# Optimization experiments

Hardware: AMD Instinct MI355X
Metric: run time of the kernel (lower is better)

## Reference

```python
import jax, jax.numpy as jnp
import numpy as np

B, S, DMODEL, HEADS = 2, 2048, 1024, 16
DK = DMODEL // HEADS
DV = DMODEL // HEADS


def setup_inputs() -> dict:
    key = jax.random.key(0)
    kx, kq, kk, kv = jax.random.split(key, 4)
    x = jax.random.normal(kx, (B, S, DMODEL), dtype=jnp.float32)
    # stacked per-head projection weights, shape [H, dmodel, dk/dv]
    # (equivalent to nn.Linear(dmodel, dk, bias=False) per head)
    scale = 1.0 / np.sqrt(DMODEL)
    Wq = jax.random.uniform(kq, (HEADS, DMODEL, DK), jnp.float32, -scale, scale)
    Wk = jax.random.uniform(kk, (HEADS, DMODEL, DK), jnp.float32, -scale, scale)
    Wv = jax.random.uniform(kv, (HEADS, DMODEL, DV), jnp.float32, -scale, scale)
    return {"x": x, "Wq": Wq, "Wk": Wk, "Wv": Wv}


def reference(x, Wq, Wk, Wv):
    # per-head projections, batched across heads: [B,H,S,dk]
    q = jnp.einsum("bsd,hdk->bhsk", x, Wq)
    k = jnp.einsum("bsd,hdk->bhsk", x, Wk)
    v = jnp.einsum("bsd,hdv->bhsv", x, Wv)
    # NOTE: original module applies NO 1/sqrt(dk) scaling — keep faithful
    scores = jnp.einsum("bhqk,bhsk->bhqs", q, k)  # [B,H,S,S]
    attn = jax.nn.softmax(scores, axis=-1)
    out = jnp.einsum("bhqs,bhsv->bhqv", attn, v)  # [B,H,S,dv]
    # concat heads along last dim in head order
    Bsz, H, Sq, Dv = out.shape
    return jnp.transpose(out, (0, 2, 1, 3)).reshape(Bsz, Sq, H * Dv)
```

## Files before the change

kernel.cpp:

```cpp
#include <hip/hip_runtime.h>

#define B_ 2
#define S_ 2048
#define D_ 1024
#define H_ 16
#define DK_ 64
#define M_ (B_ * S_)
#define N_ (3 * D_)

typedef __bf16 bf16x8 __attribute__((ext_vector_type(8)));
typedef short s8vec __attribute__((ext_vector_type(8)));
typedef float f4vec __attribute__((ext_vector_type(4)));
typedef float f16vec __attribute__((ext_vector_type(16)));

static __device__ __forceinline__ ushort f2b(float f) {
  union { float f; unsigned u; } v; v.f = f;
  unsigned u = v.u;
  u += 0x7FFFu + ((u >> 16) & 1u);
  return (ushort)(u >> 16);
}

static __device__ __forceinline__ unsigned pk2(float a, float b) {
#if __has_builtin(__builtin_amdgcn_cvt_pk_bf16_f32)
  typedef __bf16 b2 __attribute__((ext_vector_type(2)));
  b2 r = __builtin_amdgcn_cvt_pk_bf16_f32(a, b);
  return __builtin_bit_cast(unsigned, r);
#else
  return (unsigned)f2b(a) | ((unsigned)f2b(b) << 16);
#endif
}

static __device__ __forceinline__ float exp2f_fast(float x) {
#if __has_builtin(__builtin_amdgcn_exp2f)
  return __builtin_amdgcn_exp2f(x);
#else
  return __expf(x * 0.6931471805599453f);
#endif
}

static __device__ __forceinline__ f4vec mfma16(s8vec a, s8vec b, f4vec c) {
  return __builtin_amdgcn_mfma_f32_16x16x32_bf16(
      __builtin_bit_cast(bf16x8, a), __builtin_bit_cast(bf16x8, b), c, 0, 0, 0);
}

static __device__ __forceinline__ f16vec mfma32(s8vec a, s8vec b, f16vec c) {
  return __builtin_amdgcn_mfma_f32_32x32x16_bf16(
      __builtin_bit_cast(bf16x8, a), __builtin_bit_cast(bf16x8, b), c, 0, 0, 0);
}

static __device__ __forceinline__ void gl_lds16(const ushort* g, ushort* l) {
  __builtin_amdgcn_global_load_lds(
      (const __attribute__((address_space(1))) unsigned*)g,
      (__attribute__((address_space(3))) unsigned*)l, 16, 0, 0);
}

__global__ __launch_bounds__(256) void cvt_xw(const float* __restrict__ x,
                                              const float* __restrict__ Wq,
                                              const float* __restrict__ Wk,
                                              const float* __restrict__ Wv,
                                              ushort* __restrict__ xb,
                                              ushort* __restrict__ wbt) {
  __shared__ ushort T[64 * 72];
  const int t = threadIdx.x;
  if (blockIdx.x < 4096) {
    int i = blockIdx.x * 256 + t;
    float4 v = ((const float4*)x)[i];
    ushort4 o;
    o.x = f2b(v.x); o.y = f2b(v.y); o.z = f2b(v.z); o.w = f2b(v.w);
    ((ushort4*)xb)[i] = o;
    return;
  }
  const int r = blockIdx.x - 4096;
  const int w = r >> 8, h = (r >> 4) & 15, d0 = (r & 15) * 64;
  const float* W = (w == 0) ? Wq : (w == 1) ? Wk : Wv;
  const float sc = (w == 0) ? 1.4426950408889634f : 1.0f;
  const float* src = W + (size_t)h * 65536 + (size_t)d0 * 64;
#pragma unroll
  for (int j = 0; j < 4; ++j) {
    int idx = j * 256 + t;
    int dr = idx >> 4, kc = (idx & 15) * 4;
    float4 v = *(const float4*)(src + dr * 64 + kc);
    T[(kc + 0) * 72 + dr] = f2b(v.x * sc);
    T[(kc + 1) * 72 + dr] = f2b(v.y * sc);
    T[(kc + 2) * 72 + dr] = f2b(v.z * sc);
    T[(kc + 3) * 72 + dr] = f2b(v.w * sc);
  }
  __syncthreads();
  const int kk = t >> 2, dcg = (t & 3) * 16;
  ushort* dst = wbt + ((size_t)w * 1024 + h * 64 + kk) * 1024 + d0 + dcg;
  *(s8vec*)dst       = *(const s8vec*)&T[kk * 72 + dcg];
  *(s8vec*)(dst + 8) = *(const s8vec*)&T[kk * 72 + dcg + 8];
}

__global__ __launch_bounds__(512) void proj_gemm(const ushort* __restrict__ xb,
                                                 const ushort* __restrict__ wbt,
                                                 ushort* __restrict__ qkv) {
  __shared__ __attribute__((aligned(16))) ushort As[2][256 * 64];
  __shared__ __attribute__((aligned(16))) ushort Bs[2][192 * 64];
  const int tid = threadIdx.x, wid = tid >> 6, lane = tid & 63;
  const int quad = lane >> 4, l15 = lane & 15;
  const int wm = wid & 1, wn = wid >> 1;
  const int m0 = blockIdx.x * 256, n0 = blockIdx.y * 192;

  f4vec acc[8][3];
#pragma unroll
  for (int mb = 0; mb < 8; mb++)
#pragma unroll
    for (int nb = 0; nb < 3; nb++)
#pragma unroll
      for (int i = 0; i < 4; i++) acc[mb][nb][i] = 0.f;

  const int sr = tid >> 3, sg = tid & 7;
  const int gk = sg ^ (sr & 7) ^ ((sr >> 3) & 7);
  const ushort* Ab = xb + (size_t)m0 * D_;
  const ushort* Bb = wbt + (size_t)n0 * D_;

#define PSTAGE(buf, k0_)                                                    \
  do {                                                                      \
    _Pragma("unroll")                                                       \
    for (int j = 0; j < 4; ++j)                                             \
      gl_lds16(Ab + (size_t)(j * 64 + sr) * D_ + (k0_) + gk * 8,            \
               &As[buf][(j * 64 + wid * 8) * 64]);                          \
    _Pragma("unroll")                                                       \
    for (int j = 0; j < 3; ++j)                                             \
      gl_lds16(Bb + (size_t)(j * 64 + sr) * D_ + (k0_) + gk * 8,            \
               &Bs[buf][(j * 64 + wid * 8) * 64]);                          \
  } while (0)

#define PCOMP(buf)                                                          \
  do {                                                                      \
    _Pragma("unroll")                                                       \
    for (int kb = 0; kb < 2; ++kb) {                                        \
      s8vec af[8], bf[3];                                                   \
      _Pragma("unroll")                                                     \
      for (int mb = 0; mb < 8; ++mb) {                                      \
        int m = wm * 128 + mb * 16 + l15;                                   \
        int gpos = (kb * 4 + quad) ^ (m & 7) ^ ((mb * 2 + (l15 >> 3)) & 7); \
        af[mb] = *(const s8vec*)&As[buf][m * 64 + gpos * 8];                \
      }                                                                     \
      _Pragma("unroll")                                                     \
      for (int nb = 0; nb < 3; ++nb) {                                      \
        int n = wn * 48 + nb * 16 + l15;                                    \
        int gpos = (kb * 4 + quad) ^ (n & 7) ^                              \
                   ((wn * 6 + nb * 2 + (l15 >> 3)) & 7);                    \
        bf[nb] = *(const s8vec*)&Bs[buf][n * 64 + gpos * 8];                \
      }                                                                     \
      _Pragma("unroll")                                                     \
      for (int mb = 0; mb < 8; ++mb)                                        \
        _Pragma("unroll")                                                   \
        for (int nb = 0; nb < 3; ++nb)                                      \
          acc[mb][nb] = mfma16(af[mb], bf[nb], acc[mb][nb]);                \
    }                                                                       \
  } while (0)

  PSTAGE(0, 0);
  __syncthreads();
  for (int t = 0; t < 15; ++t) {
    const int cur = t & 1;
    PSTAGE(cur ^ 1, (t + 1) * 64);
    PCOMP(cur);
    __syncthreads();
  }
  PCOMP(1);
#undef PSTAGE
#undef PCOMP

  const size_t per = (size_t)B_ * H_ * S_ * DK_;
  ushort* vt = qkv + 2 * per;
#pragma unroll
  for (int mb = 0; mb < 8; ++mb)
#pragma unroll
    for (int nb = 0; nb < 3; ++nb) {
      const int n1g = n0 + wn * 48 + nb * 16 + l15;
      const int w = n1g >> 10, n1 = n1g & 1023;
      if (w == 2) {
#pragma unroll
        for (int i = 0; i < 4; ++i) {
          int m = m0 + wm * 128 + mb * 16 + quad * 4 + i;
          int b = m >> 11, s = m & 2047;
          vt[((size_t)b * 1024 + n1) * S_ + s] = f2b(acc[mb][nb][i]);
        }
      } else {
#pragma unroll
        for (int i = 0; i < 4; ++i) {
          int m = m0 + wm * 128 + mb * 16 + quad * 4 + i;
          int b = m >> 11, s = m & 2047;
          qkv[(size_t)w * per + (((size_t)b * H_ + (n1 >> 6)) * S_ + s) * 64 + (n1 & 63)] =
              f2b(acc[mb][nb][i]);
        }
      }
    }
}

__global__ __launch_bounds__(512) void attn(const ushort* __restrict__ qg,
                                            const ushort* __restrict__ kg,
                                            const ushort* __restrict__ vtg,
                                            float* __restrict__ out) {
  __shared__ __attribute__((aligned(16))) ushort POOL[2][128 * 64 + 2 * 64 * 64];
  __shared__ float LM[4][32];
  float* OM = (float*)POOL;

  const int L = blockIdx.x + (blockIdx.y << 4);
  const int orig = (L & 7) * 64 + (L >> 3);
  const int qt = orig & 15, bh = orig >> 4;
  const int b = bh >> 4, h = bh & 15;
  const int tid = threadIdx.x, wid = tid >> 6, lane = tid & 63;
  const int l31 = lane & 31, hi = lane >> 5, l7 = lane & 7;
  const int j3 = l31 >> 3;
  const int qgi = wid >> 1, kh = wid & 1;

  const ushort* qb = qg + ((size_t)bh * S_ + qt * 128 + qgi * 32) * DK_;
  s8vec bq[4];
#pragma unroll
  for (int s = 0; s < 4; ++s)
    bq[s] = *(const s8vec*)(qb + (size_t)l31 * DK_ + s * 16 + hi * 8);

  f16vec o[2];
  float lsum = 0.f;
#pragma unroll
  for (int dvh = 0; dvh < 2; ++dvh)
#pragma unroll
    for (int i = 0; i < 16; ++i) o[dvh][i] = 0.f;

  const int srow = wid * 8 + (lane >> 3);
  const int gk = (lane & 7) ^ ((lane >> 3) & 7) ^ wid;
  const ushort* kb_ = kg + (size_t)bh * S_ * DK_;
  const ushort* vb_ = vtg + (size_t)bh * 64 * S_ + (size_t)srow * S_;

#define STAGE(buf, kt_)                                                     \
  do {                                                                      \
    const ushort* kk0 = kb_ + (size_t)((kt_) * 128 + srow) * DK_ + gk * 8;  \
    gl_lds16(kk0, &POOL[buf][wid * 512]);                                   \
    gl_lds16(kk0 + (size_t)64 * DK_, &POOL[buf][4096 + wid * 512]);         \
    gl_lds16(vb_ + (kt_) * 128 + gk * 8, &POOL[buf][8192 + wid * 512]);     \
    gl_lds16(vb_ + (kt_) * 128 + 64 + gk * 8,                               \
             &POOL[buf][8192 + 4096 + wid * 512]);                          \
  } while (0)

  STAGE(0, 0);
  __syncthreads();

  for (int kt = 0; kt < S_ / 128; ++kt) {
    const int cur = kt & 1;
    if (kt + 1 < S_ / 128) STAGE(cur ^ 1, kt + 1);

    const ushort* ksb = POOL[cur];
    const ushort* vtb = POOL[cur] + 8192;
#pragma unroll
    for (int c = 0; c < 2; ++c) {
      const int row0 = kh * 64 + c * 32 + l31;
      const int akx = l7 ^ ((c * 4 + j3) & 7);
      s8vec ak[4];
#pragma unroll
      for (int s = 0; s < 4; ++s)
        ak[s] = *(const s8vec*)&ksb[row0 * 64 + ((2 * s + hi) ^ akx) * 8];

      f16vec st;
#pragma unroll
      for (int i = 0; i < 16; ++i) st[i] = 0.f;
      __builtin_amdgcn_s_setprio(1);
#pragma unroll
      for (int s = 0; s < 4; ++s) st = mfma32(ak[s], bq[s], st);
      __builtin_amdgcn_s_setprio(0);

      float p[16];
#pragma unroll
      for (int r = 0; r < 16; ++r) p[r] = exp2f_fast(st[r]);
      lsum += (((p[0] + p[1]) + (p[2] + p[3])) + ((p[4] + p[5]) + (p[6] + p[7]))) +
              (((p[8] + p[9]) + (p[10] + p[11])) + ((p[12] + p[13]) + (p[14] + p[15])));
#pragma unroll
      for (int m = 0; m < 2; ++m) {
        unsigned u01 = pk2(p[m * 8 + 0], p[m * 8 + 1]);
        unsigned u23 = pk2(p[m * 8 + 2], p[m * 8 + 3]);
        unsigned u89 = pk2(p[m * 8 + 4], p[m * 8 + 5]);
        unsigned uAB = pk2(p[m * 8 + 6], p[m * 8 + 7]);
        asm("v_permlane32_swap_b32 %0, %1" : "+v"(u01), "+v"(u89));
        asm("v_permlane32_swap_b32 %0, %1" : "+v"(u23), "+v"(uAB));
        union { unsigned u[4]; s8vec v; } pb;
        pb.u[0] = u01; pb.u[1] = u23; pb.u[2] = u89; pb.u[3] = uAB;
        __builtin_amdgcn_s_setprio(1);
#pragma unroll
        for (int dvh = 0; dvh < 2; ++dvh) {
          s8vec av = *(const s8vec*)&vtb[kh * 4096 + (dvh * 32 + l31) * 64 +
                                         (((4 * c + 2 * m + hi) ^ l7 ^
                                           ((dvh * 4 + j3) & 7)) * 8)];
          o[dvh] = mfma32(av, pb.v, o[dvh]);
        }
        __builtin_amdgcn_s_setprio(0);
      }
    }
    __syncthreads();
  }
#undef STAGE

  lsum += __shfl_xor(lsum, 32, 64);

  if (kh == 1) {
#pragma unroll
    for (int dvh = 0; dvh < 2; ++dvh)
#pragma unroll
      for (int r = 0; r < 16; ++r)
        OM[(qgi * 2 + dvh) * 2048 + r * 64 + lane] = o[dvh][r];
    if (!hi) LM[qgi][l31] = lsum;
  }
  __syncthreads();
  if (kh == 0) {
    const float linv = 1.0f / (lsum + LM[qgi][l31]);
    float* ob = out + ((size_t)b * S_ + qt * 128 + qgi * 32) * D_ + h * DK_;
#pragma unroll
    for (int dvh = 0; dvh < 2; ++dvh)
#pragma unroll
      for (int qd = 0; qd < 4; ++qd) {
        float4 vv;
        vv.x = (o[dvh][qd * 4 + 0] + OM[(qgi * 2 + dvh) * 2048 + (qd * 4 + 0) * 64 + lane]) * linv;
        vv.y = (o[dvh][qd * 4 + 1] + OM[(qgi * 2 + dvh) * 2048 + (qd * 4 + 1) * 64 + lane]) * linv;
        vv.z = (o[dvh][qd * 4 + 2] + OM[(qgi * 2 + dvh) * 2048 + (qd * 4 + 2) * 64 + lane]) * linv;
        vv.w = (o[dvh][qd * 4 + 3] + OM[(qgi * 2 + dvh) * 2048 + (qd * 4 + 3) * 64 + lane]) * linv;
        *(float4*)&ob[(size_t)l31 * D_ + dvh * 32 + qd * 8 + 4 * hi] = vv;
      }
  }
}

extern "C" void kernel_launch(void* const* d_in, const int* in_sizes, int n_in,
                              void* d_out, int out_size, void* d_ws, size_t ws_size,
                              hipStream_t stream) {
  const float* x  = (const float*)d_in[0];
  const float* Wq = (const float*)d_in[1];
  const float* Wk = (const float*)d_in[2];
  const float* Wv = (const float*)d_in[3];
  float* out = (float*)d_out;

  ushort* xb  = (ushort*)d_ws;
  ushort* wbt = xb + (size_t)B_ * S_ * D_;
  ushort* qkv = wbt + (size_t)3 * D_ * D_;
  const size_t per = (size_t)B_ * H_ * S_ * DK_;

  cvt_xw<<<4096 + 768, 256, 0, stream>>>(x, Wq, Wk, Wv, xb, wbt);
  proj_gemm<<<dim3(M_ / 256, N_ / 192), 512, 0, stream>>>(xb, wbt, qkv);
  attn<<<dim3(S_ / 128, B_ * H_), 512, 0, stream>>>(qkv, qkv + per, qkv + 2 * per, out);
}
```

Before: 164.6 us.

## Double query tile per attention block to reuse staged K/V tiles

Measured after the change: 166.0 us. Within noise of the previous version (+0.8%).

```diff
diff --git a/kernel.cpp b/kernel.cpp
--- a/kernel.cpp
+++ b/kernel.cpp
@@ -197,33 +197,37 @@
                                             const ushort* __restrict__ vtg,
                                             float* __restrict__ out) {
   __shared__ __attribute__((aligned(16))) ushort POOL[2][128 * 64 + 2 * 64 * 64];
-  __shared__ float LM[4][32];
+  __shared__ float LM[4][64];
   float* OM = (float*)POOL;
 
-  const int L = blockIdx.x + (blockIdx.y << 4);
-  const int orig = (L & 7) * 64 + (L >> 3);
-  const int qt = orig & 15, bh = orig >> 4;
+  const int L = blockIdx.x + (blockIdx.y << 3);
+  const int orig = (L & 7) * 32 + (L >> 3);
+  const int qt = orig & 7, bh = orig >> 3;
   const int b = bh >> 4, h = bh & 15;
   const int tid = threadIdx.x, wid = tid >> 6, lane = tid & 63;
   const int l31 = lane & 31, hi = lane >> 5, l7 = lane & 7;
   const int j3 = l31 >> 3;
   const int qgi = wid >> 1, kh = wid & 1;
 
-  const ushort* qb = qg + ((size_t)bh * S_ + qt * 128 + qgi * 32) * DK_;
-  s8vec bq[4];
-#pragma unroll
-  for (int s = 0; s < 4; ++s)
-    bq[s] = *(const s8vec*)(qb + (size_t)l31 * DK_ + s * 16 + hi * 8);
-
-  f16vec o[2];
-  float lsum = 0.f;
+  const ushort* qb = qg + ((size_t)bh * S_ + qt * 256 + qgi * 64) * DK_;
+  s8vec bq[2][4];
+#pragma unroll
+  for (int qs = 0; qs < 2; ++qs)
+#pragma unroll
+    for (int s = 0; s < 4; ++s)
+      bq[qs][s] = *(const s8vec*)(qb + (size_t)(qs * 32 + l31) * DK_ + s * 16 + hi * 8);
+
+  f16vec o[2][2];
+  float lsum[2] = {0.f, 0.f};
 #pragma unroll
   for (int dvh = 0; dvh < 2; ++dvh)
 #pragma unroll
-    for (int i = 0; i < 16; ++i) o[dvh][i] = 0.f;
+    for (int qs = 0; qs < 2; ++qs)
+#pragma unroll
+      for (int i = 0; i < 16; ++i) o[dvh][qs][i] = 0.f;
 
   const int srow = wid * 8 + (lane >> 3);
-  const int gk = (lane & 7) ^ ((lane >> 3) & 7) ^ wid;
+  const int gk = (lane & 7) ^ (lane >> 3) ^ wid;
   const ushort* kb_ = kg + (size_t)bh * S_ * DK_;
   const ushort* vb_ = vtg + (size_t)bh * 64 * S_ + (size_t)srow * S_;
 
@@ -255,69 +259,90 @@
       for (int s = 0; s < 4; ++s)
         ak[s] = *(const s8vec*)&ksb[row0 * 64 + ((2 * s + hi) ^ akx) * 8];
 
-      f16vec st;
-#pragma unroll
-      for (int i = 0; i < 16; ++i) st[i] = 0.f;
+      f16vec st[2];
+#pragma unroll
+      for (int qs = 0; qs < 2; ++qs)
+#pragma unroll
+        for (int i = 0; i < 16; ++i) st[qs][i] = 0.f;
       __builtin_amdgcn_s_setprio(1);
 #pragma unroll
-      for (int s = 0; s < 4; ++s) st = mfma32(ak[s], bq[s], st);
+      for (int s = 0; s < 4; ++s) {
+        st[0] = mfma32(ak[s], bq[0][s], st[0]);
+        st[1] = mfma32(ak[s], bq[1][s], st[1]);
+      }
       __builtin_amdgcn_s_setprio(0);
 
-      float p[16];
-#pragma unroll
-      for (int r = 0; r < 16; ++r) p[r] = exp2f_fast(st[r]);
-      lsum += (((p[0] + p[1]) + (p[2] + p[3])) + ((p[4] + p[5]) + (p[6] + p[7]))) +
-              (((p[8] + p[9]) + (p[10] + p[11])) + ((p[12] + p[13]) + (p[14] + p[15])));
-#pragma unroll
-      for (int m = 0; m < 2; ++m) {
-        unsigned u01 = pk2(p[m * 8 + 0], p[m * 8 + 1]);
-        unsigned u23 = pk2(p[m * 8 + 2], p[m * 8 + 3]);
-        unsigned u89 = pk2(p[m * 8 + 4], p[m * 8 + 5]);
-        unsigned uAB = pk2(p[m * 8 + 6], p[m * 8 + 7]);
-        asm("v_permlane32_swap_b32 %0, %1" : "+v"(u01), "+v"(u89));
-        asm("v_permlane32_swap_b32 %0, %1" : "+v"(u23), "+v"(uAB));
-        union { unsigned u[4]; s8vec v; } pb;
-        pb.u[0] = u01; pb.u[1] = u23; pb.u[2] = u89; pb.u[3] = uAB;
-        __builtin_amdgcn_s_setprio(1);
-#pragma unroll
-        for (int dvh = 0; dvh < 2; ++dvh) {
-          s8vec av = *(const s8vec*)&vtb[kh * 4096 + (dvh * 32 + l31) * 64 +
-                                         (((4 * c + 2 * m + hi) ^ l7 ^
-                                           ((dvh * 4 + j3) & 7)) * 8)];
-          o[dvh] = mfma32(av, pb.v, o[dvh]);
+#pragma unroll
+      for (int qs = 0; qs < 2; ++qs) {
+        float p[16];
+#pragma unroll
+        for (int r = 0; r < 16; ++r) p[r] = exp2f_fast(st[qs][r]);
+        lsum[qs] +=
+            (((p[0] + p[1]) + (p[2] + p[3])) + ((p[4] + p[5]) + (p[6] + p[7]))) +
+            (((p[8] + p[9]) + (p[10] + p[11])) + ((p[12] + p[13]) + (p[14] + p[15])));
+#pragma unroll
+        for (int m = 0; m < 2; ++m) {
+          unsigned u01 = pk2(p[m * 8 + 0], p[m * 8 + 1]);
+          unsigned u23 = pk2(p[m * 8 + 2], p[m * 8 + 3]);
+          unsigned u89 = pk2(p[m * 8 + 4], p[m * 8 + 5]);
+          unsigned uAB = pk2(p[m * 8 + 6], p[m * 8 + 7]);
+          asm("v_permlane32_swap_b32 %0, %1" : "+v"(u01), "+v"(u89));
+          asm("v_permlane32_swap_b32 %0, %1" : "+v"(u23), "+v"(uAB));
+          union { unsigned u[4]; s8vec v; } pb;
+          pb.u[0] = u01; pb.u[1] = u23; pb.u[2] = u89; pb.u[3] = uAB;
+          __builtin_amdgcn_s_setprio(1);
+#pragma unroll
+          for (int dvh = 0; dvh < 2; ++dvh) {
+            s8vec av = *(const s8vec*)&vtb[kh * 4096 + (dvh * 32 + l31) * 64 +
+                                           (((4 * c + 2 * m + hi) ^ l7 ^
+                                             ((dvh * 4 + j3) & 7)) * 8)];
+            o[dvh][qs] = mfma32(av, pb.v, o[dvh][qs]);
+          }
+          __builtin_amdgcn_s_setprio(0);
         }
-        __builtin_amdgcn_s_setprio(0);
       }
     }
     __syncthreads();
   }
 #undef STAGE
 
-  lsum += __shfl_xor(lsum, 32, 64);
+#pragma unroll
+  for (int qs = 0; qs < 2; ++qs) lsum[qs] += __shfl_xor(lsum[qs], 32, 64);
 
   if (kh == 1) {
 #pragma unroll
     for (int dvh = 0; dvh < 2; ++dvh)
 #pragma unroll
-      for (int r = 0; r < 16; ++r)
-        OM[(qgi * 2 + dvh) * 2048 + r * 64 + lane] = o[dvh][r];
-    if (!hi) LM[qgi][l31] = lsum;
+      for (int qs = 0; qs < 2; ++qs)
+#pragma unroll
+        for (int r = 0; r < 16; ++r)
+          OM[(qgi * 4 + dvh * 2 + qs) * 1024 + r * 64 + lane] = o[dvh][qs][r];
+    if (!hi) {
+      LM[qgi][l31]      = lsum[0];
+      LM[qgi][32 + l31] = lsum[1];
+    }
   }
   __syncthreads();
   if (kh == 0) {
-    const float linv = 1.0f / (lsum + LM[qgi][l31]);
-    float* ob = out + ((size_t)b * S_ + qt * 128 + qgi * 32) * D_ + h * DK_;
+    float linv[2];
+#pragma unroll
+    for (int qs = 0; qs < 2; ++qs)
+      linv[qs] = 1.0f / (lsum[qs] + LM[qgi][qs * 32 + l31]);
+    float* ob = out + ((size_t)b * S_ + qt * 256 + qgi * 64) * D_ + h * DK_;
 #pragma unroll
     for (int dvh = 0; dvh < 2; ++dvh)
 #pragma unroll
-      for (int qd = 0; qd < 4; ++qd) {
-        float4 vv;
-        vv.x = (o[dvh][qd * 4 + 0] + OM[(qgi * 2 + dvh) * 2048 + (qd * 4 + 0) * 64 + lane]) * linv;
-        vv.y = (o[dvh][qd * 4 + 1] + OM[(qgi * 2 + dvh) * 2048 + (qd * 4 + 1) * 64 + lane]) * linv;
-        vv.z = (o[dvh][qd * 4 + 2] + OM[(qgi * 2 + dvh) * 2048 + (qd * 4 + 2) * 64 + lane]) * linv;
-        vv.w = (o[dvh][qd * 4 + 3] + OM[(qgi * 2 + dvh) * 2048 + (qd * 4 + 3) * 64 + lane]) * linv;
-        *(float4*)&ob[(size_t)l31 * D_ + dvh * 32 + qd * 8 + 4 * hi] = vv;
-      }
+      for (int qs = 0; qs < 2; ++qs)
+#pragma unroll
+        for (int qd = 0; qd < 4; ++qd) {
+          const int slot = (qgi * 4 + dvh * 2 + qs) * 1024;
+          float4 vv;
+          vv.x = (o[dvh][qs][qd * 4 + 0] + OM[slot + (qd * 4 + 0) * 64 + lane]) * linv[qs];
+          vv.y = (o[dvh][qs][qd * 4 + 1] + OM[slot + (qd * 4 + 1) * 64 + lane]) * linv[qs];
+          vv.z = (o[dvh][qs][qd * 4 + 2] + OM[slot + (qd * 4 + 2) * 64 + lane]) * linv[qs];
+          vv.w = (o[dvh][qs][qd * 4 + 3] + OM[slot + (qd * 4 + 3) * 64 + lane]) * linv[qs];
+          *(float4*)&ob[(size_t)(qs * 32 + l31) * D_ + dvh * 32 + qd * 8 + 4 * hi] = vv;
+        }
   }
 }
 
@@ -337,5 +362,5 @@
 
   cvt_xw<<<4096 + 768, 256, 0, stream>>>(x, Wq, Wk, Wv, xb, wbt);
   proj_gemm<<<dim3(M_ / 256, N_ / 192), 512, 0, stream>>>(xb, wbt, qkv);
-  attn<<<dim3(S_ / 128, B_ * H_), 512, 0, stream>>>(qkv, qkv + per, qkv + 2 * per, out);
-}
+  attn<<<dim3(S_ / 256, B_ * H_), 512, 0, stream>>>(qkv, qkv + per, qkv + 2 * per, out);
+}
```
